# Performance work log

Measured on AMD Instinct MI355X. Metric: run time of the kernel, lower is better.

The kernel has to match this reference:

```python
import jax, jax.numpy as jnp
import numpy as np

N_EMBD = 1024
N_HEAD = 16
HEAD_DIM = N_EMBD // N_HEAD
EPS = 1e-5


def setup_inputs() -> dict:
    key = jax.random.key(0)
    ks = jax.random.split(key, 6)
    B, S, D = 2, 2048, N_EMBD
    s = 0.02
    return {
        "x": jax.random.normal(ks[0], (B, S, D), jnp.float32),
        "ln1_g": jnp.ones((D,), jnp.float32),
        "ln1_b": jnp.zeros((D,), jnp.float32),
        "w_attn": jax.random.normal(ks[1], (D, 3 * D), jnp.float32) * s,
        "b_attn": jnp.zeros((3 * D,), jnp.float32),
        "w_attn_proj": jax.random.normal(ks[2], (D, D), jnp.float32) * s,
        "b_attn_proj": jnp.zeros((D,), jnp.float32),
        "ln2_g": jnp.ones((D,), jnp.float32),
        "ln2_b": jnp.zeros((D,), jnp.float32),
        "w_fc": jax.random.normal(ks[3], (D, 4 * D), jnp.float32) * s,
        "b_fc": jnp.zeros((4 * D,), jnp.float32),
        "w_fc_proj": jax.random.normal(ks[4], (4 * D, D), jnp.float32) * s,
        "b_fc_proj": jnp.zeros((D,), jnp.float32),
    }


def _layernorm(x, g, b):
    mu = jnp.mean(x, axis=-1, keepdims=True)
    var = jnp.mean(jnp.square(x - mu), axis=-1, keepdims=True)
    return (x - mu) * jax.lax.rsqrt(var + EPS) * g + b


def _block(x, ln1_g, ln1_b, w_attn, b_attn, w_attn_proj, b_attn_proj,
           ln2_g, ln2_b, w_fc, b_fc, w_fc_proj, b_fc_proj):
    B, S, D = x.shape
    h = _layernorm(x, ln1_g, ln1_b)
    qkv = h @ w_attn + b_attn                       # [B,S,3D]
    q, k, v = jnp.split(qkv, 3, axis=-1)
    # [B,H,S,hd]
    q = q.reshape(B, S, N_HEAD, HEAD_DIM).transpose(0, 2, 1, 3)
    k = k.reshape(B, S, N_HEAD, HEAD_DIM).transpose(0, 2, 1, 3)
    v = v.reshape(B, S, N_HEAD, HEAD_DIM).transpose(0, 2, 1, 3)
    scores = jnp.einsum("bhqd,bhkd->bhqk", q, k) / jnp.sqrt(
        jnp.asarray(HEAD_DIM, x.dtype))
    causal = jnp.tril(jnp.ones((S, S), bool))
    scores = jnp.where(causal, scores, -jnp.inf)
    attn = jax.nn.softmax(scores, axis=-1)
    out = jnp.einsum("bhqk,bhkd->bhqd", attn, v)    # [B,H,S,hd]
    out = out.transpose(0, 2, 1, 3).reshape(B, S, D)
    x = x + (out @ w_attn_proj + b_attn_proj)
    h2 = _layernorm(x, ln2_g, ln2_b)
    m = jax.nn.gelu(h2 @ w_fc + b_fc, approximate=False)
    x = x + (m @ w_fc_proj + b_fc_proj)
    return x


def reference(x, ln1_g, ln1_b, w_attn, b_attn, w_attn_proj, b_attn_proj,
              ln2_g, ln2_b, w_fc, b_fc, w_fc_proj, b_fc_proj):
    return _block(x, ln1_g, ln1_b, w_attn, b_attn, w_attn_proj, b_attn_proj,
                  ln2_g, ln2_b, w_fc, b_fc, w_fc_proj, b_fc_proj)
```

## Files before the change

### kernel.cpp

```cpp
#include <hip/hip_runtime.h>
#include <hip/hip_bf16.h>
#include <math.h>

typedef __bf16 bf16_t;
typedef bf16_t bf16x8 __attribute__((ext_vector_type(8)));
typedef float f32x4 __attribute__((ext_vector_type(4)));
typedef unsigned short u16;
typedef u16 ushort8 __attribute__((ext_vector_type(8)));

static __device__ __forceinline__ u16 f2bf(float f) {
    unsigned u = __builtin_bit_cast(unsigned, f);
    u += 0x7FFFu + ((u >> 16) & 1u);
    return (u16)(u >> 16);
}

__global__ __launch_bounds__(256) void ln_kernel(
    const float* __restrict__ x, const float* __restrict__ g,
    const float* __restrict__ be, u16* __restrict__ out)
{
    const int row = blockIdx.x;
    const int tid = threadIdx.x;
    const float4 v = ((const float4*)(x + (long)row * 1024))[tid];
    float s = v.x + v.y + v.z + v.w;
#pragma unroll
    for (int d = 32; d >= 1; d >>= 1) s += __shfl_xor(s, d);
    __shared__ float r1[4], r2[4];
    if ((tid & 63) == 0) r1[tid >> 6] = s;
    __syncthreads();
    const float mean = (r1[0] + r1[1] + r1[2] + r1[3]) * (1.0f / 1024.0f);
    const float dx = v.x - mean, dy = v.y - mean, dz = v.z - mean, dw = v.w - mean;
    float sq = dx * dx + dy * dy + dz * dz + dw * dw;
#pragma unroll
    for (int d = 32; d >= 1; d >>= 1) sq += __shfl_xor(sq, d);
    if ((tid & 63) == 0) r2[tid >> 6] = sq;
    __syncthreads();
    const float var = (r2[0] + r2[1] + r2[2] + r2[3]) * (1.0f / 1024.0f);
    const float rstd = rsqrtf(var + 1e-5f);
    const float4 gg = ((const float4*)g)[tid];
    const float4 bb = ((const float4*)be)[tid];
    ushort4 o;
    o.x = f2bf(dx * rstd * gg.x + bb.x);
    o.y = f2bf(dy * rstd * gg.y + bb.y);
    o.z = f2bf(dz * rstd * gg.z + bb.z);
    o.w = f2bf(dw * rstd * gg.w + bb.w);
    *(ushort4*)&out[(long)row * 1024 + tid * 4] = o;
}

__global__ __launch_bounds__(256) void tcvt_kernel(
    const float* __restrict__ in, u16* __restrict__ outT, int R, int C)
{
    __shared__ float tile[32][33];
    const int tx = threadIdx.x, ty = threadIdx.y;
    const int c0 = blockIdx.x * 32, r0 = blockIdx.y * 32;
#pragma unroll
    for (int i = 0; i < 4; ++i)
        tile[ty + i * 8][tx] = in[(long)(r0 + ty + i * 8) * C + c0 + tx];
    __syncthreads();
#pragma unroll
    for (int i = 0; i < 4; ++i)
        outT[(long)(c0 + ty + i * 8) * R + r0 + tx] = f2bf(tile[tx][ty + i * 8]);
}

template <int EPI, int DP>
static __device__ __forceinline__ void gemm128_body(
    const u16* __restrict__ A, const u16* __restrict__ Bt,
    const float* __restrict__ bias, const float* __restrict__ resid,
    void* __restrict__ C, int M, int N, int K)
{
    constexpr int MR = 4, NR = 4;
    constexpr int LPW = 4;
    __shared__ __align__(16) u16 As[DP][128 * 32];
    __shared__ __align__(16) u16 Bs[DP][128 * 32];
    const int tid = threadIdx.x;
    const int lane = tid & 63;
    const int w = tid >> 6;
    const int wm = w >> 1, wn = w & 1;
    const int bm = blockIdx.x, bn = blockIdx.y;
    f32x4 acc[MR][NR] = {};

    const u16* Ablk = A + (long)bm * 128 * K;
    const u16* Bblk = Bt + (long)bn * 128 * K;
    const int nt = K >> 5;

    auto stage = [&](int buf, int kb) {
#pragma unroll
        for (int i = 0; i < 2; ++i) {
            const int o = (w * 2 + i) * 512 + lane * 8;
            const int row = o >> 5, kk = o & 31;
            __builtin_amdgcn_global_load_lds(
                (const __attribute__((address_space(1))) void*)(Ablk + (long)row * K + kb + kk),
                (__attribute__((address_space(3))) void*)(&As[buf][(w * 2 + i) * 512]),
                16, 0, 0);
            __builtin_amdgcn_global_load_lds(
                (const __attribute__((address_space(1))) void*)(Bblk + (long)row * K + kb + kk),
                (__attribute__((address_space(3))) void*)(&Bs[buf][(w * 2 + i) * 512]),
                16, 0, 0);
        }
    };

#pragma unroll
    for (int s = 0; s < DP - 1; ++s) stage(s, s << 5);

    for (int t = 0; t < nt; ++t) {
        const int cur = t % DP;
        if (t + DP - 2 < nt) {
            asm volatile("s_waitcnt vmcnt(%0)" :: "i"((DP - 2) * LPW) : "memory");
        } else if (t + 1 < nt) {
            asm volatile("s_waitcnt vmcnt(%0)" :: "i"(LPW) : "memory");
        } else {
            asm volatile("s_waitcnt vmcnt(0)" ::: "memory");
        }
        __builtin_amdgcn_s_barrier();
        asm volatile("" ::: "memory");

        if (t + DP - 1 < nt) stage((t + DP - 1) % DP, (t + DP - 1) << 5);

        bf16x8 af[MR], bfr[NR];
#pragma unroll
        for (int m = 0; m < MR; ++m)
            af[m] = *(const bf16x8*)&As[cur][(wm * 64 + m * 16 + (lane & 15)) * 32 + (lane >> 4) * 8];
#pragma unroll
        for (int n = 0; n < NR; ++n)
            bfr[n] = *(const bf16x8*)&Bs[cur][(wn * 64 + n * 16 + (lane & 15)) * 32 + (lane >> 4) * 8];
#pragma unroll
        for (int m = 0; m < MR; ++m)
#pragma unroll
            for (int n = 0; n < NR; ++n)
                acc[m][n] = __builtin_amdgcn_mfma_f32_16x16x32_bf16(af[m], bfr[n], acc[m][n], 0, 0, 0);
        asm volatile("" ::: "memory");
    }

    const int rowBase = bm * 128 + wm * 64;
    const int colBase = bn * 128 + wn * 64;
#pragma unroll
    for (int n = 0; n < NR; ++n) {
        const int col = colBase + n * 16 + (lane & 15);
        const float bv = bias[col];
#pragma unroll
        for (int m = 0; m < MR; ++m) {
#pragma unroll
            for (int r = 0; r < 4; ++r) {
                const int row = rowBase + m * 16 + (lane >> 4) * 4 + r;
                float v = acc[m][n][r] + bv;
                if constexpr (EPI == 1) {
                    const float u = v + 0.044715f * v * v * v;
                    v = v / (1.0f + __expf(-1.5957691216057308f * u));
                }
                if constexpr (EPI == 3) {
                    if (col < 1024) v *= 0.125f;
                }
                if constexpr (EPI == 2) {
                    ((float*)C)[(long)row * N + col] = v + resid[(long)row * N + col];
                } else {
                    ((u16*)C)[(long)row * N + col] = f2bf(v);
                }
            }
        }
    }
}

template <int EPI>
static __device__ __forceinline__ void gemm64_body(
    const u16* __restrict__ A, const u16* __restrict__ Bt,
    const float* __restrict__ bias, const float* __restrict__ resid,
    void* __restrict__ C, int M, int N, int K)
{
    constexpr int MR = 4, NR = 2;
    __shared__ __align__(16) u16 As[2][64 * 32];
    const int tid = threadIdx.x;
    const int lane = tid & 63;
    const int w = tid >> 6;
    const int bm = blockIdx.x, bn = blockIdx.y;
    f32x4 acc[MR][NR] = {};

    const u16* Ablk = A + (long)bm * 64 * K;
    const u16* Bblk = Bt + (long)bn * 128 * K;
    const int nt = K >> 5;

    const u16* bp0 = Bblk + (long)(w * 32 + (lane & 15)) * K + (lane >> 4) * 8;
    const u16* bp1 = bp0 + 16 * K;

    auto stageA = [&](int buf, int kb) {
        const int o = w * 512 + lane * 8;
        __builtin_amdgcn_global_load_lds(
            (const __attribute__((address_space(1))) void*)(Ablk + (long)(o >> 5) * K + kb + (o & 31)),
            (__attribute__((address_space(3))) void*)(&As[buf][w * 512]),
            16, 0, 0);
    };

    ushort8 bBa[2], bBb[2];
    stageA(0, 0);
    __builtin_amdgcn_sched_barrier(0);
    asm volatile("global_load_dwordx4 %0, %1, off" : "=v"(bBa[0]) : "v"(bp0));
    asm volatile("global_load_dwordx4 %0, %1, off" : "=v"(bBa[1]) : "v"(bp1));

    auto iter = [&](int t, ushort8* curB, ushort8* nxtB) {
        asm volatile("s_waitcnt vmcnt(2)" ::: "memory");
        __builtin_amdgcn_s_barrier();
        asm volatile("" ::: "memory");
        const bool more = (t + 1 < nt);
        if (more) {
            stageA((t + 1) & 1, (t + 1) << 5);
            __builtin_amdgcn_sched_barrier(0);
            const u16* a0 = bp0 + ((t + 1) << 5);
            const u16* a1 = bp1 + ((t + 1) << 5);
            asm volatile("global_load_dwordx4 %0, %1, off" : "=v"(nxtB[0]) : "v"(a0));
            asm volatile("global_load_dwordx4 %0, %1, off" : "=v"(nxtB[1]) : "v"(a1));
        }
        bf16x8 af[MR];
#pragma unroll
        for (int m = 0; m < MR; ++m)
            af[m] = *(const bf16x8*)&As[t & 1][(m * 16 + (lane & 15)) * 32 + (lane >> 4) * 8];
        if (more) asm volatile("s_waitcnt vmcnt(3)" ::: "memory");
        else      asm volatile("s_waitcnt vmcnt(0)" ::: "memory");
        __builtin_amdgcn_sched_barrier(0);
        const bf16x8 b0 = __builtin_bit_cast(bf16x8, curB[0]);
        const bf16x8 b1 = __builtin_bit_cast(bf16x8, curB[1]);
#pragma unroll
        for (int m = 0; m < MR; ++m) {
            acc[m][0] = __builtin_amdgcn_mfma_f32_16x16x32_bf16(af[m], b0, acc[m][0], 0, 0, 0);
            acc[m][1] = __builtin_amdgcn_mfma_f32_16x16x32_bf16(af[m], b1, acc[m][1], 0, 0, 0);
        }
        asm volatile("" ::: "memory");
    };

    for (int t = 0; t < nt; t += 2) {
        iter(t, bBa, bBb);
        iter(t + 1, bBb, bBa);
    }

    const int rowBase = bm * 64;
    const int colBase = bn * 128 + w * 32;
#pragma unroll
    for (int n = 0; n < NR; ++n) {
        const int col = colBase + n * 16 + (lane & 15);
        const float bv = bias[col];
#pragma unroll
        for (int m = 0; m < MR; ++m) {
#pragma unroll
            for (int r = 0; r < 4; ++r) {
                const int row = rowBase + m * 16 + (lane >> 4) * 4 + r;
                float v = acc[m][n][r] + bv;
                if constexpr (EPI == 1) {
                    const float u = v + 0.044715f * v * v * v;
                    v = v / (1.0f + __expf(-1.5957691216057308f * u));
                }
                if constexpr (EPI == 2) {
                    ((float*)C)[(long)row * N + col] = v + resid[(long)row * N + col];
                } else {
                    ((u16*)C)[(long)row * N + col] = f2bf(v);
                }
            }
        }
    }
}

__global__ __launch_bounds__(256) void gemm_qkv(
    const u16* A, const u16* Bt, const float* bias, const float* resid,
    void* C, int M, int N, int K) { gemm128_body<3, 3>(A, Bt, bias, resid, C, M, N, K); }
__global__ __launch_bounds__(256) void gemm_fc(
    const u16* A, const u16* Bt, const float* bias, const float* resid,
    void* C, int M, int N, int K) { gemm128_body<1, 3>(A, Bt, bias, resid, C, M, N, K); }
__global__ __launch_bounds__(256) void gemm_ap(
    const u16* A, const u16* Bt, const float* bias, const float* resid,
    void* C, int M, int N, int K) { gemm64_body<2>(A, Bt, bias, resid, C, M, N, K); }
__global__ __launch_bounds__(256) void gemm_fp(
    const u16* A, const u16* Bt, const float* bias, const float* resid,
    void* C, int M, int N, int K) { gemm64_body<2>(A, Bt, bias, resid, C, M, N, K); }

__global__ __launch_bounds__(256) void attn_kernel(
    const u16* __restrict__ qkv, u16* __restrict__ outb)
{
    const int S = 2048;
    const int flat = blockIdx.x + 16 * blockIdx.y;
    const int work = (flat & 7) * 64 + (flat >> 3);
    const int ipair = work & 15;
    const int bh = work >> 4;
    const int b = bh >> 4, h = bh & 15;
    const int tid = threadIdx.x, lane = tid & 63, w = tid >> 6;
    __shared__ __align__(16) u16 Ks[2][64 * 72];
    __shared__ __align__(16) u16 Vs[2][64 * 72];
    __shared__ __align__(16) u16 Ps[4][16 * 72];

    const long base = (long)b * S * 3072;
    const int rstage = tid >> 3;
    const int cg = (tid & 7) * 8;
    const int sw = cg;
    const u16* kbase = qkv + base + 1024 + h * 64 + cg;
    const u16* vbase = qkv + base + 2048 + h * 64 + cg;

    for (int half = 0; half < 2; ++half) {
        const int qt = half ? 31 - ipair : ipair;
        const int q0 = qt * 64;

        bf16x8 qf[2];
        {
            const int qrow = q0 + w * 16 + (lane & 15);
#pragma unroll
            for (int c = 0; c < 2; ++c)
                qf[c] = *(const bf16x8*)&qkv[base + (long)qrow * 3072 + h * 64 + c * 32 + (lane >> 4) * 8];
        }

        f32x4 Of[4] = {};
        float m = -1e30f, l = 0.0f;

        ushort8 kr[2], vr[2];
#pragma unroll
        for (int it = 0; it < 2; ++it) {
            const long ro = (long)(it * 32 + rstage) * 3072;
            kr[it] = *(const ushort8*)&kbase[ro];
            vr[it] = *(const ushort8*)&vbase[ro];
        }
        __syncthreads();
#pragma unroll
        for (int it = 0; it < 2; ++it) {
            const int r = it * 32 + rstage;
            *(ushort8*)&Ks[0][r * 72 + cg] = kr[it];
#pragma unroll
            for (int j = 0; j < 8; ++j)
                Vs[0][(cg + j) * 72 + (r ^ sw)] = vr[it][j];
        }

        for (int kt = 0; kt <= qt; ++kt) {
            const int cur = kt & 1;
            if (kt < qt) {
#pragma unroll
                for (int it = 0; it < 2; ++it) {
                    const long ro = (long)((kt + 1) * 64 + it * 32 + rstage) * 3072;
                    kr[it] = *(const ushort8*)&kbase[ro];
                    vr[it] = *(const ushort8*)&vbase[ro];
                }
            }
            __syncthreads();

            f32x4 Sf[4] = {};
#pragma unroll
            for (int f = 0; f < 4; ++f) {
#pragma unroll
                for (int c = 0; c < 2; ++c) {
                    const bf16x8 kf = *(const bf16x8*)&Ks[cur][(f * 16 + (lane & 15)) * 72 + c * 32 + (lane >> 4) * 8];
                    Sf[f] = __builtin_amdgcn_mfma_f32_16x16x32_bf16(kf, qf[c], Sf[f], 0, 0, 0);
                }
            }
            if (kt == qt) {
                const int ql = w * 16 + (lane & 15);
#pragma unroll
                for (int f = 0; f < 4; ++f) {
#pragma unroll
                    for (int r = 0; r < 4; ++r) {
                        const int kvl = f * 16 + ((lane >> 4) << 2) + r;
                        if (kvl > ql) Sf[f][r] = -1e30f;
                    }
                }
            }
            float pmax = Sf[0][0];
#pragma unroll
            for (int f = 0; f < 4; ++f)
#pragma unroll
                for (int r = 0; r < 4; ++r) pmax = fmaxf(pmax, Sf[f][r]);
            if (!__all(pmax <= m + 8.0f)) {
                float pm = pmax;
                pm = fmaxf(pm, __shfl_xor(pm, 16));
                pm = fmaxf(pm, __shfl_xor(pm, 32));
                const float mnew = fmaxf(m, pm);
                const float sc = __expf(m - mnew);
                m = mnew;
                l *= sc;
                float sco[4];
#pragma unroll
                for (int r = 0; r < 4; ++r)
                    sco[r] = __shfl(sc, ((lane >> 4) << 2) + r);
#pragma unroll
                for (int f = 0; f < 4; ++f)
#pragma unroll
                    for (int r = 0; r < 4; ++r) Of[f][r] *= sco[r];
            }
            float osum = 0.0f;
#pragma unroll
            for (int f = 0; f < 4; ++f)
#pragma unroll
                for (int r = 0; r < 4; ++r) {
                    const float e = __expf(Sf[f][r] - m);
                    Sf[f][r] = e;
                    osum += e;
                }
            l += osum;
#pragma unroll
            for (int f = 0; f < 4; ++f) {
                const unsigned lo = (unsigned)f2bf(Sf[f][0]) | ((unsigned)f2bf(Sf[f][1]) << 16);
                const unsigned hi = (unsigned)f2bf(Sf[f][2]) | ((unsigned)f2bf(Sf[f][3]) << 16);
                uint2 pk; pk.x = lo; pk.y = hi;
                *(uint2*)&Ps[w][(lane & 15) * 72 + f * 16 + ((lane >> 4) << 2)] = pk;
            }
#pragma unroll
            for (int f = 0; f < 4; ++f) {
                const int hd = f * 16 + (lane & 15);
#pragma unroll
                for (int c = 0; c < 2; ++c) {
                    const int k0 = c * 32 + (lane >> 4) * 8;
                    const bf16x8 pa = *(const bf16x8*)&Ps[w][(lane & 15) * 72 + k0];
                    const bf16x8 vb = *(const bf16x8*)&Vs[cur][hd * 72 + (k0 ^ (hd & 56))];
                    Of[f] = __builtin_amdgcn_mfma_f32_16x16x32_bf16(pa, vb, Of[f], 0, 0, 0);
                }
            }
            if (kt < qt) {
#pragma unroll
                for (int it = 0; it < 2; ++it) {
                    const int r = it * 32 + rstage;
                    *(ushort8*)&Ks[cur ^ 1][r * 72 + cg] = kr[it];
#pragma unroll
                    for (int j = 0; j < 8; ++j)
                        Vs[cur ^ 1][(cg + j) * 72 + (r ^ sw)] = vr[it][j];
                }
            }
        }

        float lt = l;
        lt += __shfl_xor(lt, 16);
        lt += __shfl_xor(lt, 32);
        const float linv = 1.0f / lt;
        float inv[4];
#pragma unroll
        for (int r = 0; r < 4; ++r)
            inv[r] = __shfl(linv, ((lane >> 4) << 2) + r);
#pragma unroll
        for (int f = 0; f < 4; ++f) {
            const int col = h * 64 + f * 16 + (lane & 15);
#pragma unroll
            for (int r = 0; r < 4; ++r) {
                const int qrow = q0 + w * 16 + (lane >> 4) * 4 + r;
                outb[((long)b * S + qrow) * 1024 + col] = f2bf(Of[f][r] * inv[r]);
            }
        }
    }
}

extern "C" void kernel_launch(void* const* d_in, const int* in_sizes, int n_in,
                              void* d_out, int out_size, void* d_ws, size_t ws_size,
                              hipStream_t stream) {
    const float* x      = (const float*)d_in[0];
    const float* ln1_g  = (const float*)d_in[1];
    const float* ln1_b  = (const float*)d_in[2];
    const float* w_attn = (const float*)d_in[3];
    const float* b_attn = (const float*)d_in[4];
    const float* w_ap   = (const float*)d_in[5];
    const float* b_ap   = (const float*)d_in[6];
    const float* ln2_g  = (const float*)d_in[7];
    const float* ln2_b  = (const float*)d_in[8];
    const float* w_fc   = (const float*)d_in[9];
    const float* b_fc   = (const float*)d_in[10];
    const float* w_fp   = (const float*)d_in[11];
    const float* b_fp   = (const float*)d_in[12];
    float* out = (float*)d_out;

    const int R = 4096;
    char* p = (char*)d_ws;
    u16*   wTa  = (u16*)(p);
    u16*   wTap = (u16*)(p + 6291456);
    u16*   wTfc = (u16*)(p + 8388608);
    u16*   wTfp = (u16*)(p + 16777216);
    u16*   hao  = (u16*)(p + 25165824);
    u16*   qkv  = (u16*)(p + 33554432);
    u16*   mb   = hao;
    u16*   h2   = wTa;
    float* x1   = out;

    const dim3 tb(32, 8);
    tcvt_kernel<<<dim3(3072 / 32, 1024 / 32), tb, 0, stream>>>(w_attn, wTa, 1024, 3072);
    tcvt_kernel<<<dim3(1024 / 32, 1024 / 32), tb, 0, stream>>>(w_ap, wTap, 1024, 1024);
    tcvt_kernel<<<dim3(4096 / 32, 1024 / 32), tb, 0, stream>>>(w_fc, wTfc, 1024, 4096);
    tcvt_kernel<<<dim3(1024 / 32, 4096 / 32), tb, 0, stream>>>(w_fp, wTfp, 4096, 1024);

    ln_kernel<<<R, 256, 0, stream>>>(x, ln1_g, ln1_b, hao);
    gemm_qkv<<<dim3(32, 24), 256, 0, stream>>>(hao, wTa, b_attn, nullptr, qkv, R, 3072, 1024);
    attn_kernel<<<dim3(16, 32), 256, 0, stream>>>(qkv, hao);
    gemm_ap<<<dim3(64, 8), 256, 0, stream>>>(hao, wTap, b_ap, x, x1, R, 1024, 1024);
    ln_kernel<<<R, 256, 0, stream>>>(x1, ln2_g, ln2_b, h2);
    gemm_fc<<<dim3(32, 32), 256, 0, stream>>>(h2, wTfc, b_fc, nullptr, mb, R, 4096, 1024);
    gemm_fp<<<dim3(64, 8), 256, 0, stream>>>(mb, wTfp, b_fp, x1, out, R, 1024, 4096);
}
```

Baseline: 271.3 us.

## Swizzle GEMM LDS tiles, triple-buffer 64-row GEMM, add setprio around attention MFMAs

Both GEMM bodies now write A/B tiles into LDS with an XOR-swizzled row/column mapping via per-lane global offsets, and read fragments back through the matching swizzle, to avoid LDS bank conflicts on the fragment reads. The 64-row GEMM used for the attention and MLP output projections moves from double to triple buffering for both the LDS A tile and the register-held B tiles, with adjusted vmcnt waits and a three-way unrolled loop, so loads are issued further ahead. The attention kernel raises wave priority around its two MFMA phases. The changes add register and LDS pressure and more complex wait accounting. The fixed two-step tail also assumes a K-tile count whose remainder after the three-way loop is exactly two.

```diff
diff --git a/kernel.cpp b/kernel.cpp
--- a/kernel.cpp
+++ b/kernel.cpp
@@ -12,6 +12,18 @@
     unsigned u = __builtin_bit_cast(unsigned, f);
     u += 0x7FFFu + ((u >> 16) & 1u);
     return (u16)(u >> 16);
+}
+
+static __device__ __forceinline__ int swz_row(int s, int lane) {
+    const int t = (lane & 7) ^ ((lane >> 3) & 7);
+    return s * 16 + ((lane >> 3) << 1) + (t >> 2);
+}
+static __device__ __forceinline__ int swz_kk(int lane) {
+    const int t = (lane & 7) ^ ((lane >> 3) & 7);
+    return (t & 3) << 3;
+}
+static __device__ __forceinline__ int swz_rd(int R, int c) {
+    return (R >> 1) * 64 + (((((R & 1) << 2) + c) ^ ((R >> 1) & 7)) << 3);
 }
 
 __global__ __launch_bounds__(256) void ln_kernel(
@@ -82,17 +94,20 @@
     const u16* Bblk = Bt + (long)bn * 128 * K;
     const int nt = K >> 5;
 
+    long soff[2];
+#pragma unroll
+    for (int i = 0; i < 2; ++i)
+        soff[i] = (long)swz_row(w * 2 + i, lane) * K + swz_kk(lane);
+
     auto stage = [&](int buf, int kb) {
 #pragma unroll
         for (int i = 0; i < 2; ++i) {
-            const int o = (w * 2 + i) * 512 + lane * 8;
-            const int row = o >> 5, kk = o & 31;
             __builtin_amdgcn_global_load_lds(
-                (const __attribute__((address_space(1))) void*)(Ablk + (long)row * K + kb + kk),
+                (const __attribute__((address_space(1))) void*)(Ablk + soff[i] + kb),
                 (__attribute__((address_space(3))) void*)(&As[buf][(w * 2 + i) * 512]),
                 16, 0, 0);
             __builtin_amdgcn_global_load_lds(
-                (const __attribute__((address_space(1))) void*)(Bblk + (long)row * K + kb + kk),
+                (const __attribute__((address_space(1))) void*)(Bblk + soff[i] + kb),
                 (__attribute__((address_space(3))) void*)(&Bs[buf][(w * 2 + i) * 512]),
                 16, 0, 0);
         }
@@ -116,12 +131,13 @@
         if (t + DP - 1 < nt) stage((t + DP - 1) % DP, (t + DP - 1) << 5);
 
         bf16x8 af[MR], bfr[NR];
+        const int c = lane >> 4;
 #pragma unroll
         for (int m = 0; m < MR; ++m)
-            af[m] = *(const bf16x8*)&As[cur][(wm * 64 + m * 16 + (lane & 15)) * 32 + (lane >> 4) * 8];
+            af[m] = *(const bf16x8*)&As[cur][swz_rd(wm * 64 + m * 16 + (lane & 15), c)];
 #pragma unroll
         for (int n = 0; n < NR; ++n)
-            bfr[n] = *(const bf16x8*)&Bs[cur][(wn * 64 + n * 16 + (lane & 15)) * 32 + (lane >> 4) * 8];
+            bfr[n] = *(const bf16x8*)&Bs[cur][swz_rd(wn * 64 + n * 16 + (lane & 15), c)];
 #pragma unroll
         for (int m = 0; m < MR; ++m)
 #pragma unroll
@@ -160,13 +176,13 @@
 }
 
 template <int EPI>
-static __device__ __forceinline__ void gemm64_body(
+static __device__ __forceinline__ void gemm64d3_body(
     const u16* __restrict__ A, const u16* __restrict__ Bt,
     const float* __restrict__ bias, const float* __restrict__ resid,
     void* __restrict__ C, int M, int N, int K)
 {
     constexpr int MR = 4, NR = 2;
-    __shared__ __align__(16) u16 As[2][64 * 32];
+    __shared__ __align__(16) u16 As[3][64 * 32];
     const int tid = threadIdx.x;
     const int lane = tid & 63;
     const int w = tid >> 6;
@@ -179,43 +195,54 @@
 
     const u16* bp0 = Bblk + (long)(w * 32 + (lane & 15)) * K + (lane >> 4) * 8;
     const u16* bp1 = bp0 + 16 * K;
+    const long soff = (long)swz_row(w, lane) * K + swz_kk(lane);
 
     auto stageA = [&](int buf, int kb) {
-        const int o = w * 512 + lane * 8;
         __builtin_amdgcn_global_load_lds(
-            (const __attribute__((address_space(1))) void*)(Ablk + (long)(o >> 5) * K + kb + (o & 31)),
+            (const __attribute__((address_space(1))) void*)(Ablk + soff + kb),
             (__attribute__((address_space(3))) void*)(&As[buf][w * 512]),
             16, 0, 0);
     };
 
-    ushort8 bBa[2], bBb[2];
+    ushort8 B0[2], B1[2], B2[2];
     stageA(0, 0);
     __builtin_amdgcn_sched_barrier(0);
-    asm volatile("global_load_dwordx4 %0, %1, off" : "=v"(bBa[0]) : "v"(bp0));
-    asm volatile("global_load_dwordx4 %0, %1, off" : "=v"(bBa[1]) : "v"(bp1));
-
-    auto iter = [&](int t, ushort8* curB, ushort8* nxtB) {
-        asm volatile("s_waitcnt vmcnt(2)" ::: "memory");
+    asm volatile("global_load_dwordx4 %0, %1, off" : "=v"(B0[0]) : "v"(bp0));
+    asm volatile("global_load_dwordx4 %0, %1, off" : "=v"(B0[1]) : "v"(bp1));
+    __builtin_amdgcn_sched_barrier(0);
+    stageA(1, 32);
+    __builtin_amdgcn_sched_barrier(0);
+    {
+        const u16* a0 = bp0 + 32;
+        const u16* a1 = bp1 + 32;
+        asm volatile("global_load_dwordx4 %0, %1, off" : "=v"(B1[0]) : "v"(a0));
+        asm volatile("global_load_dwordx4 %0, %1, off" : "=v"(B1[1]) : "v"(a1));
+    }
+
+    auto iter = [&](int t, int cb, int pb, ushort8 (&cur)[2], ushort8 (&pf)[2]) {
+        if (t + 1 < nt) asm volatile("s_waitcnt vmcnt(5)" ::: "memory");
+        else            asm volatile("s_waitcnt vmcnt(2)" ::: "memory");
         __builtin_amdgcn_s_barrier();
         asm volatile("" ::: "memory");
-        const bool more = (t + 1 < nt);
-        if (more) {
-            stageA((t + 1) & 1, (t + 1) << 5);
+        if (t + 2 < nt) {
+            stageA(pb, (t + 2) << 5);
             __builtin_amdgcn_sched_barrier(0);
-            const u16* a0 = bp0 + ((t + 1) << 5);
-            const u16* a1 = bp1 + ((t + 1) << 5);
-            asm volatile("global_load_dwordx4 %0, %1, off" : "=v"(nxtB[0]) : "v"(a0));
-            asm volatile("global_load_dwordx4 %0, %1, off" : "=v"(nxtB[1]) : "v"(a1));
+            const u16* a0 = bp0 + ((t + 2) << 5);
+            const u16* a1 = bp1 + ((t + 2) << 5);
+            asm volatile("global_load_dwordx4 %0, %1, off" : "=v"(pf[0]) : "v"(a0));
+            asm volatile("global_load_dwordx4 %0, %1, off" : "=v"(pf[1]) : "v"(a1));
         }
         bf16x8 af[MR];
+        const int c = lane >> 4;
 #pragma unroll
         for (int m = 0; m < MR; ++m)
-            af[m] = *(const bf16x8*)&As[t & 1][(m * 16 + (lane & 15)) * 32 + (lane >> 4) * 8];
-        if (more) asm volatile("s_waitcnt vmcnt(3)" ::: "memory");
-        else      asm volatile("s_waitcnt vmcnt(0)" ::: "memory");
+            af[m] = *(const bf16x8*)&As[cb][swz_rd(m * 16 + (lane & 15), c)];
+        if (t + 2 < nt)      asm volatile("s_waitcnt vmcnt(6)" ::: "memory");
+        else if (t + 1 < nt) asm volatile("s_waitcnt vmcnt(3)" ::: "memory");
+        else                 asm volatile("s_waitcnt vmcnt(0)" ::: "memory");
         __builtin_amdgcn_sched_barrier(0);
-        const bf16x8 b0 = __builtin_bit_cast(bf16x8, curB[0]);
-        const bf16x8 b1 = __builtin_bit_cast(bf16x8, curB[1]);
+        const bf16x8 b0 = __builtin_bit_cast(bf16x8, cur[0]);
+        const bf16x8 b1 = __builtin_bit_cast(bf16x8, cur[1]);
 #pragma unroll
         for (int m = 0; m < MR; ++m) {
             acc[m][0] = __builtin_amdgcn_mfma_f32_16x16x32_bf16(af[m], b0, acc[m][0], 0, 0, 0);
@@ -224,10 +251,14 @@
         asm volatile("" ::: "memory");
     };
 
-    for (int t = 0; t < nt; t += 2) {
-        iter(t, bBa, bBb);
-        iter(t + 1, bBb, bBa);
+    int t = 0;
+    for (; t < nt - 2; t += 3) {
+        iter(t,     0, 2, B0, B2);
+        iter(t + 1, 1, 0, B1, B0);
+        iter(t + 2, 2, 1, B2, B1);
     }
+    iter(nt - 2, 0, 2, B0, B2);
+    iter(nt - 1, 1, 0, B1, B0);
 
     const int rowBase = bm * 64;
     const int colBase = bn * 128 + w * 32;
@@ -263,10 +294,10 @@
     void* C, int M, int N, int K) { gemm128_body<1, 3>(A, Bt, bias, resid, C, M, N, K); }
 __global__ __launch_bounds__(256) void gemm_ap(
     const u16* A, const u16* Bt, const float* bias, const float* resid,
-    void* C, int M, int N, int K) { gemm64_body<2>(A, Bt, bias, resid, C, M, N, K); }
+    void* C, int M, int N, int K) { gemm64d3_body<2>(A, Bt, bias, resid, C, M, N, K); }
 __global__ __launch_bounds__(256) void gemm_fp(
     const u16* A, const u16* Bt, const float* bias, const float* resid,
-    void* C, int M, int N, int K) { gemm64_body<2>(A, Bt, bias, resid, C, M, N, K); }
+    void* C, int M, int N, int K) { gemm64d3_body<2>(A, Bt, bias, resid, C, M, N, K); }
 
 __global__ __launch_bounds__(256) void attn_kernel(
     const u16* __restrict__ qkv, u16* __restrict__ outb)
@@ -334,6 +365,7 @@
             __syncthreads();
 
             f32x4 Sf[4] = {};
+            __builtin_amdgcn_s_setprio(1);
 #pragma unroll
             for (int f = 0; f < 4; ++f) {
 #pragma unroll
@@ -342,6 +374,7 @@
                     Sf[f] = __builtin_amdgcn_mfma_f32_16x16x32_bf16(kf, qf[c], Sf[f], 0, 0, 0);
                 }
             }
+            __builtin_amdgcn_s_setprio(0);
             if (kt == qt) {
                 const int ql = w * 16 + (lane & 15);
 #pragma unroll
@@ -392,6 +425,7 @@
                 uint2 pk; pk.x = lo; pk.y = hi;
                 *(uint2*)&Ps[w][(lane & 15) * 72 + f * 16 + ((lane >> 4) << 2)] = pk;
             }
+            __builtin_amdgcn_s_setprio(1);
 #pragma unroll
             for (int f = 0; f < 4; ++f) {
                 const int hd = f * 16 + (lane & 15);
@@ -403,6 +437,7 @@
                     Of[f] = __builtin_amdgcn_mfma_f32_16x16x32_bf16(pa, vb, Of[f], 0, 0, 0);
                 }
             }
+            __builtin_amdgcn_s_setprio(0);
             if (kt < qt) {
 #pragma unroll
                 for (int it = 0; it < 2; ++it) {
```

Measured after the change: 264.1 us. -2.6%, faster.
